# Kernel optimization log

Measured on AMD Instinct MI355X. Metric: run time of the kernel, lower is better.

## Reference

```python
import jax, jax.numpy as jnp
import numpy as np

B, N, F, U, NH = 1, 4096, 32, 32, 2
NEG = -1e10


def _leaky(x):
    # tf.nn.leaky_relu default alpha = 0.2
    return jnp.where(x >= 0, x, 0.2 * x)


def setup_inputs() -> dict:
    key = jax.random.key(0)
    k = jax.random.split(key, 6)
    H_r = jax.random.normal(k[0], (B, N, F), dtype=jnp.float32)
    H_i = jax.random.normal(k[1], (B, N, F), dtype=jnp.float32)
    # sparse-ish adjacency with self loops, stored dense as the module expects
    adj = (jax.random.uniform(k[2], (B, N, N)) < 0.005).astype(jnp.float32)
    A = jnp.maximum(adj, jnp.eye(N, dtype=jnp.float32)[None])
    s_w = float(np.sqrt(6.0 / (F + U)))
    s_a = float(np.sqrt(6.0 / (U + 1)))
    W = jax.random.uniform(k[3], (NH, F, U), minval=-s_w, maxval=s_w, dtype=jnp.float32)
    a1 = jax.random.uniform(k[4], (NH, U), minval=-s_a, maxval=s_a, dtype=jnp.float32)
    a2 = jax.random.uniform(k[5], (NH, U), minval=-s_a, maxval=s_a, dtype=jnp.float32)
    return {"H_r": H_r, "H_i": H_i, "A": A, "W": W, "a1": a1, "a2": a2}


def reference(H_r, H_i, A, W, a1, a2):
    # complex X = H @ W  (W real): decompose into real/imag, vectorized over heads
    Xr = jnp.einsum('bnf,hfu->hbnu', H_r, W)   # [NH,B,N,U]
    Xi = jnp.einsum('bnf,hfu->hbnu', H_i, W)
    # additive attention logits: self + neighbours^T
    sr = jnp.einsum('hbnu,hu->hbn', Xr, a1)
    si = jnp.einsum('hbnu,hu->hbn', Xi, a1)
    nr = jnp.einsum('hbnu,hu->hbn', Xr, a2)
    ni = jnp.einsum('hbnu,hu->hbn', Xi, a2)
    E1 = _leaky(sr[..., :, None] + nr[..., None, :])   # [NH,B,N,N]
    E2 = _leaky(si[..., :, None] + ni[..., None, :])
    mask = NEG * (1.0 - A)                              # [B,N,N], broadcasts over heads
    alpha1 = jax.nn.softmax(E1 + mask, axis=-1)
    alpha2 = jax.nn.softmax(E2 + mask, axis=-1)
    # complex alpha @ complex X
    Hr_cap = jnp.einsum('hbij,hbju->hbiu', alpha1, Xr) - jnp.einsum('hbij,hbju->hbiu', alpha2, Xi)
    Hi_cap = jnp.einsum('hbij,hbju->hbiu', alpha1, Xi) + jnp.einsum('hbij,hbju->hbiu', alpha2, Xr)
    # concat heads on feature dim (output_layer=False, activation=identity)
    out_r = jnp.transpose(Hr_cap, (1, 2, 0, 3)).reshape(B, N, NH * U)
    out_i = jnp.transpose(Hi_cap, (1, 2, 0, 3)).reshape(B, N, NH * U)
    return (out_r, out_i)
```

## Files before the change

kernel.cpp:

```cpp
#include <hip/hip_runtime.h>
#include <math.h>

namespace {
constexpr int N  = 4096;
constexpr int F  = 32;
constexpr int U  = 32;
constexpr int NH = 2;

__device__ __forceinline__ float leaky(float x) {
    return x >= 0.f ? x : 0.2f * x;
}

__global__ __launch_bounds__(256) void proj_kernel(
    const float* __restrict__ Hr, const float* __restrict__ Hi,
    const float* __restrict__ W,  const float* __restrict__ a1,
    const float* __restrict__ a2,
    float2* __restrict__ Xp, float2* __restrict__ Sp, float2* __restrict__ Np)
{
    __shared__ float sW[NH * F * U];
    __shared__ float sH[2][8][F];
    const int t = threadIdx.x;
    for (int k = t; k < NH * F * U; k += 256) sW[k] = W[k];
    const int row0 = blockIdx.x * 8;
    {
        const int r = t >> 5, f = t & 31;
        sH[0][r][f] = Hr[(row0 + r) * F + f];
        sH[1][r][f] = Hi[(row0 + r) * F + f];
    }
    __syncthreads();

    const int r = t >> 5, u = t & 31;
    const int n = row0 + r;
    float xr[NH] = {0.f, 0.f}, xi[NH] = {0.f, 0.f};
    #pragma unroll
    for (int h = 0; h < NH; ++h) {
        #pragma unroll
        for (int f = 0; f < F; ++f) {
            const float w = sW[h * F * U + f * U + u];
            xr[h] += sH[0][r][f] * w;
            xi[h] += sH[1][r][f] * w;
        }
    }
    #pragma unroll
    for (int h = 0; h < NH; ++h)
        Xp[(h * N + n) * U + u] = make_float2(xr[h], xi[h]);

    #pragma unroll
    for (int h = 0; h < NH; ++h) {
        const float av1 = a1[h * U + u], av2 = a2[h * U + u];
        float vsr = xr[h] * av1, vnr = xr[h] * av2;
        float vsi = xi[h] * av1, vni = xi[h] * av2;
        #pragma unroll
        for (int m = 16; m; m >>= 1) {
            vsr += __shfl_xor(vsr, m, 32);
            vnr += __shfl_xor(vnr, m, 32);
            vsi += __shfl_xor(vsi, m, 32);
            vni += __shfl_xor(vni, m, 32);
        }
        if (u == 0) {
            Sp[h * N + n] = make_float2(vsr, vsi);
            Np[h * N + n] = make_float2(vnr, vni);
        }
    }
}

__global__ __launch_bounds__(256) void attn_kernel(
    const float* __restrict__ A,
    const float2* __restrict__ Xp, const float2* __restrict__ Sp,
    const float2* __restrict__ Np,
    float* __restrict__ out)
{
    __shared__ int s_idx[4][128];

    const int wv   = threadIdx.x >> 6;
    const int lane = threadIdx.x & 63;
    const int i    = blockIdx.x * 4 + wv;
    const int h    = lane >> 5;
    const int u    = lane & 31;

    const float4* __restrict__ Arow = (const float4*)(A + (size_t)i * N);
    float4 av[16];
    #pragma unroll
    for (int c = 0; c < 16; ++c) av[c] = Arow[c * 64 + lane];

    const unsigned long long lt = (1ull << lane) - 1ull;
    int cnt = 0;
    #pragma unroll
    for (int c = 0; c < 16; ++c) {
        #pragma unroll
        for (int cc = 0; cc < 4; ++cc) {
            const float vv = (cc == 0) ? av[c].x : (cc == 1) ? av[c].y
                           : (cc == 2) ? av[c].z : av[c].w;
            const unsigned long long mk = __ballot(vv != 0.f);
            if (vv != 0.f) {
                const int pos = cnt + __popcll(mk & lt);
                if (pos < 128) s_idx[wv][pos] = c * 256 + 4 * lane + cc;
            }
            cnt += __popcll(mk);
        }
    }
    if (cnt > 128) cnt = 128;
    __syncthreads();

    const float2 s = Sp[h * N + i];
    const float2* __restrict__ NpH = Np + h * N;
    const float2* __restrict__ XpH = Xp + (size_t)h * N * U;
    const int* __restrict__ idx = s_idx[wv];

    float l1 = 0.f, l2 = 0.f;
    float a1r = 0.f, a1i = 0.f, a2r = 0.f, a2i = 0.f;

    int nj = idx[0];
    float2 nn = NpH[nj];
    float2 x  = XpH[(size_t)nj * U + u];
    #pragma unroll 1
    for (int j = 0; j < cnt; ++j) {
        const float2 nn_c = nn;
        const float2 x_c  = x;
        if (j + 1 < cnt) {
            nj = idx[j + 1];
            nn = NpH[nj];
            x  = XpH[(size_t)nj * U + u];
        }
        const float w1 = __expf(leaky(s.x + nn_c.x));
        const float w2 = __expf(leaky(s.y + nn_c.y));
        l1 += w1;
        l2 += w2;
        a1r += w1 * x_c.x;
        a1i += w1 * x_c.y;
        a2r += w2 * x_c.x;
        a2i += w2 * x_c.y;
    }
    const float r1 = 1.f / l1, r2 = 1.f / l2;
    out[(size_t)i * (NH * U) + lane]                      = a1r * r1 - a2i * r2;
    out[(size_t)N * NH * U + (size_t)i * (NH * U) + lane] = a1i * r1 + a2r * r2;
}
}

extern "C" void kernel_launch(void* const* d_in, const int* in_sizes, int n_in,
                              void* d_out, int out_size, void* d_ws, size_t ws_size,
                              hipStream_t stream) {
    (void)in_sizes; (void)n_in; (void)out_size; (void)ws_size;
    const float* Hr = (const float*)d_in[0];
    const float* Hi = (const float*)d_in[1];
    const float* A  = (const float*)d_in[2];
    const float* W  = (const float*)d_in[3];
    const float* a1 = (const float*)d_in[4];
    const float* a2 = (const float*)d_in[5];
    float* out = (float*)d_out;

    float2* ws = (float2*)d_ws;
    float2* Xp = ws;
    float2* Sp = Xp + NH * N * U;
    float2* Np = Sp + NH * N;

    proj_kernel<<<N / 8, 256, 0, stream>>>(Hr, Hi, W, a1, a2, Xp, Sp, Np);
    attn_kernel<<<N / 4, 256, 0, stream>>>(A, Xp, Sp, Np, out);
}
```

Measured before the change: 117.8 us.

## Interleave heads in workspace layout and gather neighbours four at a time

Stores the projected features as node-major with both heads interleaved, so a single 64-lane row gather covers both heads in one contiguous 512-byte access. The neighbour loop is unrolled by four, with int4 index loads and four gathers prefetched one group ahead. Out-of-range slots in the last group are padded with self-indices and masked to zero weight. Also vectorizes the W staging copy and adds an occupancy launch bound, at the cost of more registers and some wasted lanes in the final group.

New measurement: 112.0 us. 1.05x faster.

```diff
diff --git a/kernel.cpp b/kernel.cpp
--- a/kernel.cpp
+++ b/kernel.cpp
@@ -20,7 +20,12 @@
     __shared__ float sW[NH * F * U];
     __shared__ float sH[2][8][F];
     const int t = threadIdx.x;
-    for (int k = t; k < NH * F * U; k += 256) sW[k] = W[k];
+    {
+        const float4* __restrict__ W4 = (const float4*)W;
+        float4* __restrict__ sW4 = (float4*)sW;
+        sW4[t]       = W4[t];
+        sW4[t + 256] = W4[t + 256];
+    }
     const int row0 = blockIdx.x * 8;
     {
         const int r = t >> 5, f = t & 31;
@@ -43,7 +48,7 @@
     }
     #pragma unroll
     for (int h = 0; h < NH; ++h)
-        Xp[(h * N + n) * U + u] = make_float2(xr[h], xi[h]);
+        Xp[((size_t)n * NH + h) * U + u] = make_float2(xr[h], xi[h]);
 
     #pragma unroll
     for (int h = 0; h < NH; ++h) {
@@ -58,30 +63,45 @@
             vni += __shfl_xor(vni, m, 32);
         }
         if (u == 0) {
-            Sp[h * N + n] = make_float2(vsr, vsi);
-            Np[h * N + n] = make_float2(vnr, vni);
+            Sp[n * NH + h] = make_float2(vsr, vsi);
+            Np[n * NH + h] = make_float2(vnr, vni);
         }
     }
 }
 
-__global__ __launch_bounds__(256) void attn_kernel(
+__device__ __forceinline__ void nb_acc(bool valid, float2 sv, float2 nnc, float2 xc,
+                                       float& l1, float& l2,
+                                       float& a1r, float& a1i,
+                                       float& a2r, float& a2i)
+{
+    float w1 = __expf(leaky(sv.x + nnc.x));
+    float w2 = __expf(leaky(sv.y + nnc.y));
+    w1 = valid ? w1 : 0.f;
+    w2 = valid ? w2 : 0.f;
+    l1 += w1; l2 += w2;
+    a1r += w1 * xc.x; a1i += w1 * xc.y;
+    a2r += w2 * xc.x; a2i += w2 * xc.y;
+}
+
+__global__ __launch_bounds__(256, 4) void attn_kernel(
     const float* __restrict__ A,
     const float2* __restrict__ Xp, const float2* __restrict__ Sp,
     const float2* __restrict__ Np,
     float* __restrict__ out)
 {
-    __shared__ int s_idx[4][128];
+    __shared__ int s_idx[4][136];
 
     const int wv   = threadIdx.x >> 6;
     const int lane = threadIdx.x & 63;
     const int i    = blockIdx.x * 4 + wv;
     const int h    = lane >> 5;
-    const int u    = lane & 31;
 
     const float4* __restrict__ Arow = (const float4*)(A + (size_t)i * N);
     float4 av[16];
     #pragma unroll
     for (int c = 0; c < 16; ++c) av[c] = Arow[c * 64 + lane];
+
+    const float2 s = Sp[i * NH + h];
 
     const unsigned long long lt = (1ull << lane) - 1ull;
     int cnt = 0;
@@ -100,37 +120,45 @@
         }
     }
     if (cnt > 128) cnt = 128;
+    if (lane < 3) s_idx[wv][cnt + lane] = i;
     __syncthreads();
 
-    const float2 s = Sp[h * N + i];
-    const float2* __restrict__ NpH = Np + h * N;
-    const float2* __restrict__ XpH = Xp + (size_t)h * N * U;
     const int* __restrict__ idx = s_idx[wv];
+    const int4* __restrict__ idx4 = (const int4*)idx;
 
     float l1 = 0.f, l2 = 0.f;
     float a1r = 0.f, a1i = 0.f, a2r = 0.f, a2i = 0.f;
+    const int ng = (cnt + 3) >> 2;
 
-    int nj = idx[0];
-    float2 nn = NpH[nj];
-    float2 x  = XpH[(size_t)nj * U + u];
+    int4 ia = idx4[0];
+    int4 ib = idx4[1];
+    float2 n0 = Np[ia.x * NH + h], n1 = Np[ia.y * NH + h];
+    float2 n2 = Np[ia.z * NH + h], n3 = Np[ia.w * NH + h];
+    float2 x0 = Xp[(size_t)ia.x * (NH * U) + lane];
+    float2 x1 = Xp[(size_t)ia.y * (NH * U) + lane];
+    float2 x2 = Xp[(size_t)ia.z * (NH * U) + lane];
+    float2 x3 = Xp[(size_t)ia.w * (NH * U) + lane];
+
     #pragma unroll 1
-    for (int j = 0; j < cnt; ++j) {
-        const float2 nn_c = nn;
-        const float2 x_c  = x;
-        if (j + 1 < cnt) {
-            nj = idx[j + 1];
-            nn = NpH[nj];
-            x  = XpH[(size_t)nj * U + u];
+    for (int g = 0; g < ng; ++g) {
+        const float2 c0 = n0, c1 = n1, c2 = n2, c3 = n3;
+        const float2 z0 = x0, z1 = x1, z2 = x2, z3 = x3;
+        const int jb = g * 4;
+        if (g + 1 < ng) {
+            n0 = Np[ib.x * NH + h]; n1 = Np[ib.y * NH + h];
+            n2 = Np[ib.z * NH + h]; n3 = Np[ib.w * NH + h];
+            x0 = Xp[(size_t)ib.x * (NH * U) + lane];
+            x1 = Xp[(size_t)ib.y * (NH * U) + lane];
+            x2 = Xp[(size_t)ib.z * (NH * U) + lane];
+            x3 = Xp[(size_t)ib.w * (NH * U) + lane];
+            ib = idx4[(g + 2 < ng) ? (g + 2) : (g + 1)];
         }
-        const float w1 = __expf(leaky(s.x + nn_c.x));
-        const float w2 = __expf(leaky(s.y + nn_c.y));
-        l1 += w1;
-        l2 += w2;
-        a1r += w1 * x_c.x;
-        a1i += w1 * x_c.y;
-        a2r += w2 * x_c.x;
-        a2i += w2 * x_c.y;
+        nb_acc(jb + 0 < cnt, s, c0, z0, l1, l2, a1r, a1i, a2r, a2i);
+        nb_acc(jb + 1 < cnt, s, c1, z1, l1, l2, a1r, a1i, a2r, a2i);
+        nb_acc(jb + 2 < cnt, s, c2, z2, l1, l2, a1r, a1i, a2r, a2i);
+        nb_acc(jb + 3 < cnt, s, c3, z3, l1, l2, a1r, a1i, a2r, a2i);
     }
+
     const float r1 = 1.f / l1, r2 = 1.f / l2;
     out[(size_t)i * (NH * U) + lane]                      = a1r * r1 - a2i * r2;
     out[(size_t)N * NH * U + (size_t)i * (NH * U) + lane] = a1i * r1 + a2r * r2;
@@ -151,8 +179,8 @@
 
     float2* ws = (float2*)d_ws;
     float2* Xp = ws;
-    float2* Sp = Xp + NH * N * U;
-    float2* Np = Sp + NH * N;
+    float2* Sp = Xp + (size_t)N * NH * U;
+    float2* Np = Sp + (size_t)N * NH;
 
     proj_kernel<<<N / 8, 256, 0, stream>>>(Hr, Hi, W, a1, a2, Xp, Sp, Np);
     attn_kernel<<<N / 4, 256, 0, stream>>>(A, Xp, Sp, Np, out);
```
